# Kernel tuning notes

Measured on AMD Instinct MI355X. Metric: run time of the kernel, lower is better.

## Reference

```python
import jax, jax.numpy as jnp
import numpy as np

OUT_FEATURES = 4096
IN_FEATURES = 4096
NNZ = 838860
N_COLS = 8192


def setup_inputs() -> dict:
    key = jax.random.key(0)
    k_r, k_c, k_v, k_x = jax.random.split(key, 4)
    rows = jax.random.randint(k_r, (NNZ,), 0, OUT_FEATURES, dtype=jnp.int32)
    cols = jax.random.randint(k_c, (NNZ,), 0, IN_FEATURES, dtype=jnp.int32)
    vals = jax.random.normal(k_v, (NNZ,), dtype=jnp.float32)
    x = jax.random.normal(k_x, (IN_FEATURES, N_COLS), dtype=jnp.float32)
    return {"rows": rows, "cols": cols, "vals": vals, "x": x}


def reference(rows, cols, vals, x):
    # Sparse COO weight W[out, in]; duplicate (row, col) entries sum, matching
    # uncoalesced COO semantics of torch.sparse.mm.
    # Dense scatter + GEMM is the clean, efficient jax expression of the same math.
    W = jnp.zeros((OUT_FEATURES, IN_FEATURES), dtype=vals.dtype).at[rows, cols].add(vals)
    return W @ x  # [out_features, N]
```

## Files before the change

kernel.cpp:

```cpp
#include <hip/hip_runtime.h>

#define OUT_F 4096
#define IN_F  4096
#define NCOLS 8192

#define GM OUT_F
#define GK IN_F
#define GN NCOLS

typedef __attribute__((ext_vector_type(8))) short short8;
typedef __attribute__((ext_vector_type(4))) float f32x4;

__device__ inline unsigned short f2bf(float f) {
    union { float f; unsigned u; } c; c.f = f;
    unsigned u = c.u;
    u += 0x7fffu + ((u >> 16) & 1u);
    return (unsigned short)(u >> 16);
}

__device__ inline void gll16(const void* g, void* l) {
    __builtin_amdgcn_global_load_lds(
        (const __attribute__((address_space(1))) unsigned int*)g,
        (__attribute__((address_space(3))) unsigned int*)l, 16, 0, 0);
}

__global__ void scatter_dense(const int* __restrict__ rows, const int* __restrict__ cols,
                              const float* __restrict__ vals, float* __restrict__ W, int nnz) {
    int i = blockIdx.x * blockDim.x + threadIdx.x;
    if (i < nnz) atomicAdd(&W[(size_t)rows[i] * IN_F + cols[i]], vals[i]);
}

__global__ void convert_w(const float* __restrict__ Wf, unsigned short* __restrict__ Wb) {
    int i = blockIdx.x * blockDim.x + threadIdx.x;
    float4 v = ((const float4*)Wf)[i];
    ushort4 o;
    o.x = f2bf(v.x); o.y = f2bf(v.y); o.z = f2bf(v.z); o.w = f2bf(v.w);
    ((ushort4*)Wb)[i] = o;
}

__global__ __launch_bounds__(256) void transpose_x(const float* __restrict__ x,
                                                   unsigned short* __restrict__ xT) {
    __shared__ float tile[64][65];
    const int k0 = blockIdx.x * 64;
    const int n0 = blockIdx.y * 64;
    const int t = threadIdx.x;
    const int c4 = (t & 15) * 4;
    const int r0 = t >> 4;
    for (int p = 0; p < 4; ++p) {
        int r = r0 + p * 16;
        float4 v = *(const float4*)&x[(size_t)(k0 + r) * NCOLS + n0 + c4];
        tile[r][c4 + 0] = v.x; tile[r][c4 + 1] = v.y;
        tile[r][c4 + 2] = v.z; tile[r][c4 + 3] = v.w;
    }
    __syncthreads();
    const int n  = t >> 2;
    const int ks = (t & 3) * 16;
    unsigned w[8];
    for (int m = 0; m < 8; ++m) {
        unsigned short lo = f2bf(tile[ks + 2 * m + 0][n]);
        unsigned short hi = f2bf(tile[ks + 2 * m + 1][n]);
        w[m] = (unsigned)lo | ((unsigned)hi << 16);
    }
    uint4* dst = (uint4*)&xT[(size_t)(n0 + n) * GK + k0 + ks];
    dst[0] = make_uint4(w[0], w[1], w[2], w[3]);
    dst[1] = make_uint4(w[4], w[5], w[6], w[7]);
}

__global__ __launch_bounds__(512, 2) void gemm256(const unsigned short* __restrict__ A,
                                                  const unsigned short* __restrict__ BT,
                                                  float* __restrict__ C) {
    __shared__ unsigned short lds[65536];

    const int tid  = threadIdx.x;
    const int wave = tid >> 6;
    const int lane = tid & 63;

    const int wg  = blockIdx.y * 32 + blockIdx.x;
    const int swz = (wg & 7) * 64 + (wg >> 3);
    const int m0  = (swz >> 5) * 256;
    const int n0  = (swz & 31) * 256;

    const int wm = wave >> 2;
    const int wn = wave & 3;

    const int r0s  = tid >> 2;
    const int swz0 = ((tid & 3) ^ ((r0s >> 1) & 3)) << 3;
    const unsigned short* pA0 = A  + (size_t)(m0 + r0s) * GK + swz0;
    const unsigned short* pA1 = pA0 + (size_t)128 * GK;
    const unsigned short* pB0 = BT + (size_t)(n0 + r0s) * GK + swz0;
    const unsigned short* pB1 = pB0 + (size_t)128 * GK;

    const int frow  = lane & 15;
    const int ajb   = ((lane >> 4) ^ ((frow >> 1) & 3)) << 3;
    const int abase = ((wm << 7) + frow) * 32 + ajb;
    const int bbase = ((wn << 6) + frow) * 32 + ajb;

    f32x4 acc[8][4] = {};

#define STAGE(q_, s_) do {                                              \
        const int ko_ = (((q_) & 127) << 5);                            \
        gll16(pA0 + ko_, &lds[(s_) * 8192 + (wave << 9)]);              \
        gll16(pA1 + ko_, &lds[(s_) * 8192 + 4096 + (wave << 9)]);       \
        gll16(pB0 + ko_, &lds[32768 + (s_) * 8192 + (wave << 9)]);      \
        gll16(pB1 + ko_, &lds[32768 + (s_) * 8192 + 4096 + (wave << 9)]); \
    } while (0)

    STAGE(0, 0); STAGE(1, 1); STAGE(2, 2);
    asm volatile("s_waitcnt vmcnt(8)");
    __builtin_amdgcn_s_barrier();

    short8 bfX[4], afX[4], bfY[4], afY[4];
    {
        const unsigned short* Ar0 = &lds[0];
        const unsigned short* Br0 = &lds[32768];
#pragma unroll
        for (int nj = 0; nj < 4; ++nj) bfX[nj] = *(const short8*)&Br0[bbase + nj * 512];
#pragma unroll
        for (int mi = 0; mi < 4; ++mi) afX[mi] = *(const short8*)&Ar0[abase + mi * 512];
    }

#define PHASE(e_, bfC, afC, bfN, afN, jj) do {                                  \
        asm volatile("s_waitcnt vmcnt(4)");                                     \
        __builtin_amdgcn_s_barrier();                                           \
        const unsigned short* ArC = &lds[(e_) * 8192];                          \
        const unsigned short* ArN = &lds[(((e_) + 1) & 3) * 8192];              \
        const unsigned short* BrN = &lds[32768 + (((e_) + 1) & 3) * 8192];      \
        short8 af2[4];                                                          \
        _Pragma("unroll")                                                       \
        for (int mi = 0; mi < 4; ++mi)                                          \
            af2[mi] = *(const short8*)&ArC[abase + (4 + mi) * 512];             \
        _Pragma("unroll")                                                       \
        for (int nj = 0; nj < 4; ++nj)                                          \
            bfN[nj] = *(const short8*)&BrN[bbase + nj * 512];                   \
        _Pragma("unroll")                                                       \
        for (int mi = 0; mi < 4; ++mi)                                          \
            afN[mi] = *(const short8*)&ArN[abase + mi * 512];                   \
        STAGE(4 * (jj) + (e_) + 3, ((e_) + 3) & 3);                             \
        __builtin_amdgcn_s_setprio(1);                                          \
        _Pragma("unroll")                                                       \
        for (int mi = 0; mi < 4; ++mi)                                          \
            _Pragma("unroll")                                                   \
            for (int nj = 0; nj < 4; ++nj)                                      \
                acc[mi][nj] = __builtin_amdgcn_mfma_f32_16x16x32_bf16(          \
                    afC[mi], bfC[nj], acc[mi][nj], 0, 0, 0);                    \
        _Pragma("unroll")                                                       \
        for (int mi = 0; mi < 4; ++mi)                                          \
            _Pragma("unroll")                                                   \
            for (int nj = 0; nj < 4; ++nj)                                      \
                acc[4 + mi][nj] = __builtin_amdgcn_mfma_f32_16x16x32_bf16(      \
                    af2[mi], bfC[nj], acc[4 + mi][nj], 0, 0, 0);                \
        __builtin_amdgcn_s_setprio(0);                                          \
    } while (0)

#pragma unroll 1
    for (int j = 0; j < GK / 128; ++j) {
        PHASE(0, bfX, afX, bfY, afY, j);
        PHASE(1, bfY, afY, bfX, afX, j);
        PHASE(2, bfX, afX, bfY, afY, j);
        PHASE(3, bfY, afY, bfX, afX, j);
    }
#undef PHASE
#undef STAGE

    for (int mi = 0; mi < 8; ++mi) {
        const int r0w = m0 + wm * 128 + mi * 16 + (lane >> 4) * 4;
        for (int nj = 0; nj < 4; ++nj) {
            const int cc = n0 + wn * 64 + nj * 16 + frow;
            for (int r = 0; r < 4; ++r)
                C[(size_t)(r0w + r) * GN + cc] = acc[mi][nj][r];
        }
    }
}

#define WS_COUNTS  0
#define WS_OFFSETS 4097
#define WS_CURSOR  8194
#define WS_HEADER  12290

__global__ void hist_kernel(const int* __restrict__ rows, int* __restrict__ counts, int nnz) {
    int i = blockIdx.x * blockDim.x + threadIdx.x;
    if (i < nnz) atomicAdd(&counts[rows[i]], 1);
}

__global__ void scan_kernel(const int* __restrict__ counts, int* __restrict__ offsets) {
    __shared__ int lsum[256];
    int t = threadIdx.x;
    int base = t * 16;
    int local[16];
    int s = 0;
    for (int i = 0; i < 16; ++i) { local[i] = counts[base + i]; s += local[i]; }
    lsum[t] = s;
    __syncthreads();
    if (t == 0) {
        int acc = 0;
        for (int i = 0; i < 256; ++i) { int v = lsum[i]; lsum[i] = acc; acc += v; }
        offsets[OUT_F] = acc;
    }
    __syncthreads();
    int acc = lsum[t];
    for (int i = 0; i < 16; ++i) { offsets[base + i] = acc; acc += local[i]; }
}

__global__ void scatter_kernel(const int* __restrict__ rows, const int* __restrict__ cols,
                               const float* __restrict__ vals,
                               const int* __restrict__ offsets, int* __restrict__ cursor,
                               int* __restrict__ cols_s, float* __restrict__ vals_s, int nnz) {
    int i = blockIdx.x * blockDim.x + threadIdx.x;
    if (i < nnz) {
        int r = rows[i];
        int pos = offsets[r] + atomicAdd(&cursor[r], 1);
        cols_s[pos] = cols[i];
        vals_s[pos] = vals[i];
    }
}

__global__ __launch_bounds__(256) void spmm_kernel(const int* __restrict__ offsets,
                                                   const int* __restrict__ cols_s,
                                                   const float* __restrict__ vals_s,
                                                   const float* __restrict__ x,
                                                   float* __restrict__ out) {
    const int row  = blockIdx.x;
    const int col0 = blockIdx.y * 1024 + threadIdx.x * 4;
    const int k0 = offsets[row];
    const int k1 = offsets[row + 1];
    float4 acc = make_float4(0.f, 0.f, 0.f, 0.f);
    for (int k = k0; k < k1; ++k) {
        const int   c = cols_s[k];
        const float v = vals_s[k];
        const float4 xv = *reinterpret_cast<const float4*>(x + (size_t)c * NCOLS + col0);
        acc.x += v * xv.x;
        acc.y += v * xv.y;
        acc.z += v * xv.z;
        acc.w += v * xv.w;
    }
    *reinterpret_cast<float4*>(out + (size_t)row * NCOLS + col0) = acc;
}

extern "C" void kernel_launch(void* const* d_in, const int* in_sizes, int n_in,
                              void* d_out, int out_size, void* d_ws, size_t ws_size,
                              hipStream_t stream) {
    const int*   rows = (const int*)d_in[0];
    const int*   cols = (const int*)d_in[1];
    const float* vals = (const float*)d_in[2];
    const float* x    = (const float*)d_in[3];
    float*       out  = (float*)d_out;
    const int nnz = in_sizes[0];

    const size_t WF_BYTES = (size_t)GM * GK * 4;
    const size_t WB_BYTES = (size_t)GM * GK * 2;
    const size_t NEED = WF_BYTES + WB_BYTES;

    if (ws_size >= NEED) {
        float*          Wf = (float*)d_ws;
        unsigned short* Wb = (unsigned short*)((char*)d_ws + WF_BYTES);
        unsigned short* xT = (unsigned short*)d_ws;

        hipMemsetAsync(Wf, 0, WF_BYTES, stream);
        scatter_dense<<<(nnz + 255) / 256, 256, 0, stream>>>(rows, cols, vals, Wf, nnz);
        convert_w<<<(GM * GK / 4) / 256, 256, 0, stream>>>(Wf, Wb);
        dim3 tg(GK / 64, GN / 64);
        transpose_x<<<tg, 256, 0, stream>>>(x, xT);
        dim3 gg(GN / 256, GM / 256);
        gemm256<<<gg, 512, 0, stream>>>(Wb, xT, out);
    } else {
        int*   ws_i    = (int*)d_ws;
        int*   counts  = ws_i + WS_COUNTS;
        int*   offsets = ws_i + WS_OFFSETS;
        int*   cursor  = ws_i + WS_CURSOR;
        int*   cols_s  = ws_i + WS_HEADER;
        float* vals_s  = (float*)(ws_i + WS_HEADER + nnz);

        hipMemsetAsync(d_ws, 0, (size_t)WS_HEADER * sizeof(int), stream);
        const int nblk = (nnz + 255) / 256;
        hist_kernel<<<nblk, 256, 0, stream>>>(rows, counts, nnz);
        scan_kernel<<<1, 256, 0, stream>>>(counts, offsets);
        scatter_kernel<<<nblk, 256, 0, stream>>>(rows, cols, vals, offsets, cursor,
                                                 cols_s, vals_s, nnz);
        dim3 grid(OUT_F, NCOLS / 1024);
        spmm_kernel<<<grid, 256, 0, stream>>>(offsets, cols_s, vals_s, x, out);
    }
}
```

Measured before the change: 531.3 us.

## Restructure bf16 GEMM main loop into K=64 double-buffered tiles with barrier-split MFMA phases

The dense bf16 GEMM mainloop moves from a 4-stage K=32 ring to 2-buffer K=64 tiles. It uses a new 8-way XOR LDS swizzle, splits each tile into four MFMA quarters separated by workgroup barriers, and remaps workgroups to tiles based on XCD index. The intent is to improve L2 locality across XCDs and reduce the number of pipeline phases, following a ping-pong style schedule. In exchange it adds many more barriers per tile, waits on vmcnt(0) every tile and keeps less prefetch depth, which can stall on global-load latency.

```diff
diff --git a/kernel.cpp b/kernel.cpp
--- a/kernel.cpp
+++ b/kernel.cpp
@@ -75,92 +75,101 @@
     const int wave = tid >> 6;
     const int lane = tid & 63;
 
-    const int wg  = blockIdx.y * 32 + blockIdx.x;
-    const int swz = (wg & 7) * 64 + (wg >> 3);
-    const int m0  = (swz >> 5) * 256;
-    const int n0  = (swz & 31) * 256;
-
+    const int wg   = blockIdx.y * 32 + blockIdx.x;
+    const int xcd  = wg & 7;
+    const int ii   = wg >> 3;
+    const int m0   = ((((ii & 7) << 1) | (xcd & 1))) << 8;
+    const int n0   = ((((ii >> 3) << 2) | ((xcd >> 1) & 3))) << 8;
     const int wm = wave >> 2;
     const int wn = wave & 3;
 
-    const int r0s  = tid >> 2;
-    const int swz0 = ((tid & 3) ^ ((r0s >> 1) & 3)) << 3;
-    const unsigned short* pA0 = A  + (size_t)(m0 + r0s) * GK + swz0;
-    const unsigned short* pA1 = pA0 + (size_t)128 * GK;
-    const unsigned short* pB0 = BT + (size_t)(n0 + r0s) * GK + swz0;
-    const unsigned short* pB1 = pB0 + (size_t)128 * GK;
-
-    const int frow  = lane & 15;
-    const int ajb   = ((lane >> 4) ^ ((frow >> 1) & 3)) << 3;
-    const int abase = ((wm << 7) + frow) * 32 + ajb;
-    const int bbase = ((wn << 6) + frow) * 32 + ajb;
+    const int sb = ((tid & 7) ^ ((tid >> 3) & 7)) << 3;
+    const unsigned short* pAs = A  + (size_t)(m0 + (tid >> 3)) * GK + sb;
+    const unsigned short* pBs = BT + (size_t)(n0 + (tid >> 3)) * GK + sb;
+
+    const int frow = lane & 15;
+    const int jhi  = lane >> 4;
+    const int so0  = ((jhi ^ (frow & 7)) << 3) + frow * 64;
+    const int so1  = (((4 | jhi) ^ (frow & 7)) << 3) + frow * 64;
+    const int ab   = (wn & 1) << 12;
 
     f32x4 acc[8][4] = {};
 
-#define STAGE(q_, s_) do {                                              \
-        const int ko_ = (((q_) & 127) << 5);                            \
-        gll16(pA0 + ko_, &lds[(s_) * 8192 + (wave << 9)]);              \
-        gll16(pA1 + ko_, &lds[(s_) * 8192 + 4096 + (wave << 9)]);       \
-        gll16(pB0 + ko_, &lds[32768 + (s_) * 8192 + (wave << 9)]);      \
-        gll16(pB1 + ko_, &lds[32768 + (s_) * 8192 + 4096 + (wave << 9)]); \
+#define REGION(c_, op_, h_) ((((((c_) << 1) | (op_)) << 1) | (h_)) << 13)
+
+#define STG(c_, op_, h_, T_) do {                                               \
+        const unsigned short* _p = ((op_) ? pBs : pAs)                          \
+                                   + (size_t)((h_) * 128) * GK + ((T_) << 6);   \
+        gll16(_p,                  &lds[REGION(c_, op_, h_) + (wave << 9)]);    \
+        gll16(_p + (size_t)64 * GK, &lds[REGION(c_, op_, h_) + 4096 + (wave << 9)]); \
     } while (0)
 
-    STAGE(0, 0); STAGE(1, 1); STAGE(2, 2);
-    asm volatile("s_waitcnt vmcnt(8)");
-    __builtin_amdgcn_s_barrier();
-
-    short8 bfX[4], afX[4], bfY[4], afY[4];
-    {
-        const unsigned short* Ar0 = &lds[0];
-        const unsigned short* Br0 = &lds[32768];
-#pragma unroll
-        for (int nj = 0; nj < 4; ++nj) bfX[nj] = *(const short8*)&Br0[bbase + nj * 512];
-#pragma unroll
-        for (int mi = 0; mi < 4; ++mi) afX[mi] = *(const short8*)&Ar0[abase + mi * 512];
-    }
-
-#define PHASE(e_, bfC, afC, bfN, afN, jj) do {                                  \
-        asm volatile("s_waitcnt vmcnt(4)");                                     \
-        __builtin_amdgcn_s_barrier();                                           \
-        const unsigned short* ArC = &lds[(e_) * 8192];                          \
-        const unsigned short* ArN = &lds[(((e_) + 1) & 3) * 8192];              \
-        const unsigned short* BrN = &lds[32768 + (((e_) + 1) & 3) * 8192];      \
-        short8 af2[4];                                                          \
-        _Pragma("unroll")                                                       \
-        for (int mi = 0; mi < 4; ++mi)                                          \
-            af2[mi] = *(const short8*)&ArC[abase + (4 + mi) * 512];             \
-        _Pragma("unroll")                                                       \
-        for (int nj = 0; nj < 4; ++nj)                                          \
-            bfN[nj] = *(const short8*)&BrN[bbase + nj * 512];                   \
-        _Pragma("unroll")                                                       \
-        for (int mi = 0; mi < 4; ++mi)                                          \
-            afN[mi] = *(const short8*)&ArN[abase + mi * 512];                   \
-        STAGE(4 * (jj) + (e_) + 3, ((e_) + 3) & 3);                             \
+#define MFMA16(H_)                                                              \
         __builtin_amdgcn_s_setprio(1);                                          \
         _Pragma("unroll")                                                       \
         for (int mi = 0; mi < 4; ++mi)                                          \
             _Pragma("unroll")                                                   \
             for (int nj = 0; nj < 4; ++nj)                                      \
-                acc[mi][nj] = __builtin_amdgcn_mfma_f32_16x16x32_bf16(          \
-                    afC[mi], bfC[nj], acc[mi][nj], 0, 0, 0);                    \
-        _Pragma("unroll")                                                       \
-        for (int mi = 0; mi < 4; ++mi)                                          \
-            _Pragma("unroll")                                                   \
-            for (int nj = 0; nj < 4; ++nj)                                      \
-                acc[4 + mi][nj] = __builtin_amdgcn_mfma_f32_16x16x32_bf16(      \
-                    af2[mi], bfC[nj], acc[4 + mi][nj], 0, 0, 0);                \
-        __builtin_amdgcn_s_setprio(0);                                          \
+                acc[(H_) * 4 + mi][nj] = __builtin_amdgcn_mfma_f32_16x16x32_bf16( \
+                    af[mi], bf[nj], acc[(H_) * 4 + mi][nj], 0, 0, 0);           \
+        __builtin_amdgcn_s_setprio(0);
+
+#define KTILE(c_, cn_, T_) do {                                                 \
+        const int Ab = (((c_) << 2) | wm) << 13;                                \
+        const int Bb = (((((c_) << 1) | 1) << 1) | (wn >> 1)) << 13;            \
+        short8 bf[4], af[4];                                                    \
+                                                                 \
+        _Pragma("unroll")                                                       \
+        for (int nj = 0; nj < 4; ++nj)                                          \
+            bf[nj] = *(const short8*)&lds[Bb + ab + nj * 1024 + so0];           \
+        _Pragma("unroll")                                                       \
+        for (int mi = 0; mi < 4; ++mi)                                          \
+            af[mi] = *(const short8*)&lds[Ab + mi * 1024 + so0];                \
+        STG(cn_, 0, 0, T_); STG(cn_, 0, 1, T_);                                 \
+        __builtin_amdgcn_s_barrier();                                           \
+        MFMA16(0)                                                               \
+        __builtin_amdgcn_s_barrier();                                           \
+                                                                 \
+        _Pragma("unroll")                                                       \
+        for (int mi = 0; mi < 4; ++mi)                                          \
+            af[mi] = *(const short8*)&lds[Ab + 4096 + mi * 1024 + so0];         \
+        STG(cn_, 1, 0, T_); STG(cn_, 1, 1, T_);                                 \
+        __builtin_amdgcn_s_barrier();                                           \
+        MFMA16(1)                                                               \
+        __builtin_amdgcn_s_barrier();                                           \
+                                                                 \
+        _Pragma("unroll")                                                       \
+        for (int nj = 0; nj < 4; ++nj)                                          \
+            bf[nj] = *(const short8*)&lds[Bb + ab + nj * 1024 + so1];           \
+        _Pragma("unroll")                                                       \
+        for (int mi = 0; mi < 4; ++mi)                                          \
+            af[mi] = *(const short8*)&lds[Ab + mi * 1024 + so1];                \
+        __builtin_amdgcn_s_barrier();                                           \
+        MFMA16(0)                                                               \
+        __builtin_amdgcn_s_barrier();                                           \
+                                                                 \
+        _Pragma("unroll")                                                       \
+        for (int mi = 0; mi < 4; ++mi)                                          \
+            af[mi] = *(const short8*)&lds[Ab + 4096 + mi * 1024 + so1];         \
+        asm volatile("s_waitcnt vmcnt(0)");                                     \
+        __builtin_amdgcn_s_barrier();                                           \
+        MFMA16(1)                                                               \
+        __builtin_amdgcn_s_barrier();                                           \
     } while (0)
 
+    STG(0, 0, 0, 0); STG(0, 0, 1, 0); STG(0, 1, 0, 0); STG(0, 1, 1, 0);
+    asm volatile("s_waitcnt vmcnt(0)");
+    __builtin_amdgcn_s_barrier();
+
 #pragma unroll 1
-    for (int j = 0; j < GK / 128; ++j) {
-        PHASE(0, bfX, afX, bfY, afY, j);
-        PHASE(1, bfY, afY, bfX, afX, j);
-        PHASE(2, bfX, afX, bfY, afY, j);
-        PHASE(3, bfY, afY, bfX, afX, j);
-    }
-#undef PHASE
-#undef STAGE
+    for (int t2 = 0; t2 < GK / 128; ++t2) {
+        KTILE(0, 1, 2 * t2 + 1);
+        KTILE(1, 0, (2 * t2 + 2) & 63);
+    }
+#undef KTILE
+#undef MFMA16
+#undef STG
+#undef REGION
 
     for (int mi = 0; mi < 8; ++mi) {
         const int r0w = m0 + wm * 128 + mi * 16 + (lane >> 4) * 4;
```

Result: faster. 504.6 us (-5.0%).

## Simplify GEMM LDS pipeline and remap workgroups to tiles per XCD

Applied to the files above, without the earlier changes.

Changes the workgroup-to-tile mapping so that each XCD covers a 2x4 patch of output tiles, aiming to improve L2 reuse of A and B panels. The LDS layout is interleaved so that each stage holds its A and B tiles contiguously. The register double-buffered fragment prefetch is replaced by loading all fragments from the current stage at the start of each phase. A second barrier per phase is added, which removes the prefetch overlap and may expose LDS read latency before the MFMAs.

```diff
diff --git a/kernel.cpp b/kernel.cpp
--- a/kernel.cpp
+++ b/kernel.cpp
@@ -75,11 +75,11 @@
     const int wave = tid >> 6;
     const int lane = tid & 63;
 
-    const int wg  = blockIdx.y * 32 + blockIdx.x;
-    const int swz = (wg & 7) * 64 + (wg >> 3);
-    const int m0  = (swz >> 5) * 256;
-    const int n0  = (swz & 31) * 256;
-
+    const int wg   = blockIdx.y * 32 + blockIdx.x;
+    const int xcd  = wg & 7;
+    const int ii   = wg >> 3;
+    const int m0   = ((((ii & 7) << 1) | (xcd & 1))) << 8;
+    const int n0   = ((((ii >> 3) << 2) | ((xcd >> 1) & 3))) << 8;
     const int wm = wave >> 2;
     const int wn = wave & 3;
 
@@ -92,72 +92,61 @@
 
     const int frow  = lane & 15;
     const int ajb   = ((lane >> 4) ^ ((frow >> 1) & 3)) << 3;
-    const int abase = ((wm << 7) + frow) * 32 + ajb;
-    const int bbase = ((wn << 6) + frow) * 32 + ajb;
+    const int abase = (((wm << 7) + frow) << 5) + ajb;
+    const int bbase = (((wn << 6) + frow) << 5) + 8192 + ajb;
 
     f32x4 acc[8][4] = {};
 
-#define STAGE(q_, s_) do {                                              \
-        const int ko_ = (((q_) & 127) << 5);                            \
-        gll16(pA0 + ko_, &lds[(s_) * 8192 + (wave << 9)]);              \
-        gll16(pA1 + ko_, &lds[(s_) * 8192 + 4096 + (wave << 9)]);       \
-        gll16(pB0 + ko_, &lds[32768 + (s_) * 8192 + (wave << 9)]);      \
-        gll16(pB1 + ko_, &lds[32768 + (s_) * 8192 + 4096 + (wave << 9)]); \
+#define STAGE(T_, s_) do {                                              \
+        const int ko_ = ((T_) & 127) << 5;                              \
+        gll16(pA0 + ko_, &lds[(s_) * 16384 + (wave << 9)]);             \
+        gll16(pA1 + ko_, &lds[(s_) * 16384 + 4096 + (wave << 9)]);      \
+        gll16(pB0 + ko_, &lds[(s_) * 16384 + 8192 + (wave << 9)]);      \
+        gll16(pB1 + ko_, &lds[(s_) * 16384 + 12288 + (wave << 9)]);     \
     } while (0)
 
     STAGE(0, 0); STAGE(1, 1); STAGE(2, 2);
     asm volatile("s_waitcnt vmcnt(8)");
     __builtin_amdgcn_s_barrier();
 
-    short8 bfX[4], afX[4], bfY[4], afY[4];
-    {
-        const unsigned short* Ar0 = &lds[0];
-        const unsigned short* Br0 = &lds[32768];
-#pragma unroll
-        for (int nj = 0; nj < 4; ++nj) bfX[nj] = *(const short8*)&Br0[bbase + nj * 512];
-#pragma unroll
-        for (int mi = 0; mi < 4; ++mi) afX[mi] = *(const short8*)&Ar0[abase + mi * 512];
-    }
-
-#define PHASE(e_, bfC, afC, bfN, afN, jj) do {                                  \
-        asm volatile("s_waitcnt vmcnt(4)");                                     \
+#define PHASE(e_, jj) do {                                                      \
+        const unsigned short* Ar = &lds[(e_) * 16384];                          \
+        short8 bf[4], af[4], af2[4];                                            \
+        _Pragma("unroll")                                                       \
+        for (int nj = 0; nj < 4; ++nj)                                          \
+            bf[nj] = *(const short8*)&Ar[bbase + nj * 512];                     \
+        _Pragma("unroll")                                                       \
+        for (int mi = 0; mi < 4; ++mi)                                          \
+            af[mi] = *(const short8*)&Ar[abase + mi * 512];                     \
+        _Pragma("unroll")                                                       \
+        for (int mi = 0; mi < 4; ++mi)                                          \
+            af2[mi] = *(const short8*)&Ar[abase + 2048 + mi * 512];             \
+        STAGE(4 * (jj) + (e_) + 3, ((e_) + 3) & 3);                             \
+        asm volatile("s_waitcnt vmcnt(8)");                                     \
         __builtin_amdgcn_s_barrier();                                           \
-        const unsigned short* ArC = &lds[(e_) * 8192];                          \
-        const unsigned short* ArN = &lds[(((e_) + 1) & 3) * 8192];              \
-        const unsigned short* BrN = &lds[32768 + (((e_) + 1) & 3) * 8192];      \
-        short8 af2[4];                                                          \
-        _Pragma("unroll")                                                       \
-        for (int mi = 0; mi < 4; ++mi)                                          \
-            af2[mi] = *(const short8*)&ArC[abase + (4 + mi) * 512];             \
-        _Pragma("unroll")                                                       \
-        for (int nj = 0; nj < 4; ++nj)                                          \
-            bfN[nj] = *(const short8*)&BrN[bbase + nj * 512];                   \
-        _Pragma("unroll")                                                       \
-        for (int mi = 0; mi < 4; ++mi)                                          \
-            afN[mi] = *(const short8*)&ArN[abase + mi * 512];                   \
-        STAGE(4 * (jj) + (e_) + 3, ((e_) + 3) & 3);                             \
         __builtin_amdgcn_s_setprio(1);                                          \
         _Pragma("unroll")                                                       \
         for (int mi = 0; mi < 4; ++mi)                                          \
             _Pragma("unroll")                                                   \
             for (int nj = 0; nj < 4; ++nj)                                      \
                 acc[mi][nj] = __builtin_amdgcn_mfma_f32_16x16x32_bf16(          \
-                    afC[mi], bfC[nj], acc[mi][nj], 0, 0, 0);                    \
+                    af[mi], bf[nj], acc[mi][nj], 0, 0, 0);                      \
         _Pragma("unroll")                                                       \
         for (int mi = 0; mi < 4; ++mi)                                          \
             _Pragma("unroll")                                                   \
             for (int nj = 0; nj < 4; ++nj)                                      \
                 acc[4 + mi][nj] = __builtin_amdgcn_mfma_f32_16x16x32_bf16(      \
-                    af2[mi], bfC[nj], acc[4 + mi][nj], 0, 0, 0);                \
+                    af2[mi], bf[nj], acc[4 + mi][nj], 0, 0, 0);                 \
         __builtin_amdgcn_s_setprio(0);                                          \
+        __builtin_amdgcn_s_barrier();                                           \
     } while (0)
 
 #pragma unroll 1
     for (int j = 0; j < GK / 128; ++j) {
-        PHASE(0, bfX, afX, bfY, afY, j);
-        PHASE(1, bfY, afY, bfX, afX, j);
-        PHASE(2, bfX, afX, bfY, afY, j);
-        PHASE(3, bfY, afY, bfX, afX, j);
+        PHASE(0, j);
+        PHASE(1, j);
+        PHASE(2, j);
+        PHASE(3, j);
     }
 #undef PHASE
 #undef STAGE
```

Measured after the change: 501.7 us. 5.6% less time.
